# Optimization experiments

Hardware: AMD Instinct MI355X
Metric: run time of the kernel (lower is better)

Reference implementation:

```python
import jax, jax.numpy as jnp
import numpy as np

N = 1_000_000
DIM = 128
NUM_GRAPHS = 4096


def setup_inputs() -> dict:
    key = jax.random.key(0)
    kx, kq, kb = jax.random.split(key, 3)
    x = jax.random.normal(kx, (N, DIM), dtype=jnp.float32)
    query = jax.random.normal(kq, (DIM,), dtype=jnp.float32) * 0.02
    batch = jnp.sort(jax.random.randint(kb, (N,), 0, NUM_GRAPHS, dtype=jnp.int64))
    return {"x": x, "query": query, "batch": batch}


def reference(x, query, batch):
    # scores: [N] dot of each node feature with the learned query vector
    scores = jnp.einsum("nd,d->n", x, query)
    # segment-wise numerically-stable softmax over nodes belonging to each graph
    seg_max = jax.ops.segment_max(scores, batch, num_segments=NUM_GRAPHS)
    ex = jnp.exp(scores - seg_max[batch])  # [N]
    seg_sum = jax.ops.segment_sum(ex, batch, num_segments=NUM_GRAPHS)
    weights = ex / seg_sum[batch]  # [N]
    # weighted scatter-add pooling -> [num_graphs, dim]
    pooled = jax.ops.segment_sum(weights[:, None] * x, batch, num_segments=NUM_GRAPHS)
    return pooled
```

## Files before the change

kernel.cpp:

```cpp
#include <hip/hip_runtime.h>
#include <math.h>

#define DIM 128
#define CHUNK 4
#define STREAMS 8
#define STRIDE (STREAMS)
#define ROUND (STREAMS * CHUNK)

__device__ __forceinline__ int lower_bound_i(const int* __restrict__ b, int n, int key) {
    int lo = 0, hi = n;
    while (lo < hi) {
        int mid = (lo + hi) >> 1;
        if (b[mid] < key) lo = mid + 1; else hi = mid;
    }
    return lo;
}

__global__ __launch_bounds__(256) void attnpool_kernel(
    const float* __restrict__ x, const float* __restrict__ q,
    const int* __restrict__ batch, float* __restrict__ out, int n)
{
    const int g    = blockIdx.x;
    const int tid  = threadIdx.x;
    const int wave = tid >> 6;
    const int lane = tid & 63;
    const int half = lane >> 5;
    const int hl   = lane & 31;
    const int sid  = wave * 2 + half;

    const int lo = lower_bound_i(batch, n, g);
    const int hi = lower_bound_i(batch, n, g + 1);

    const float4 qf = *(const float4*)(q + hl * 4);

    float  m = -INFINITY;
    float  l = 0.f;
    float4 o = make_float4(0.f, 0.f, 0.f, 0.f);

    const int i0 = lo + sid;
    const float4 z = make_float4(0.f, 0.f, 0.f, 0.f);

    float4 cur[CHUNK];
    #pragma unroll
    for (int j = 0; j < CHUNK; ++j) {
        const int ii = i0 + j * STRIDE;
        cur[j] = (ii < hi) ? *(const float4*)(x + (size_t)ii * DIM + hl * 4) : z;
    }

    for (int base = i0; base < hi; base += ROUND) {
        float4 nxt[CHUNK];
        #pragma unroll
        for (int j = 0; j < CHUNK; ++j) {
            const int ii = base + ROUND + j * STRIDE;
            nxt[j] = (ii < hi) ? *(const float4*)(x + (size_t)ii * DIM + hl * 4) : z;
        }

        float s[CHUNK];
        #pragma unroll
        for (int j = 0; j < CHUNK; ++j)
            s[j] = cur[j].x * qf.x + cur[j].y * qf.y + cur[j].z * qf.z + cur[j].w * qf.w;

        #pragma unroll
        for (int d = 16; d >= 1; d >>= 1) {
            #pragma unroll
            for (int j = 0; j < CHUNK; ++j)
                s[j] += __shfl_xor(s[j], d);
        }

        #pragma unroll
        for (int j = 0; j < CHUNK; ++j)
            if (base + j * STRIDE >= hi) s[j] = -INFINITY;

        const float smax = fmaxf(fmaxf(s[0], s[1]), fmaxf(s[2], s[3]));
        if (smax > m) {
            const float a = __expf(m - smax);
            l *= a;
            o.x *= a; o.y *= a; o.z *= a; o.w *= a;
            m = smax;
        }

        #pragma unroll
        for (int j = 0; j < CHUNK; ++j) {
            const float p = (base + j * STRIDE < hi) ? __expf(s[j] - m) : 0.f;
            l += p;
            o.x += p * cur[j].x; o.y += p * cur[j].y;
            o.z += p * cur[j].z; o.w += p * cur[j].w;
        }

        #pragma unroll
        for (int j = 0; j < CHUNK; ++j) cur[j] = nxt[j];
    }

    __shared__ float sm_m[STREAMS];
    __shared__ float sm_l[STREAMS];
    __shared__ float sm_o[STREAMS * DIM];
    if (hl == 0) { sm_m[sid] = m; sm_l[sid] = l; }
    *(float4*)(sm_o + sid * DIM + hl * 4) = o;
    __syncthreads();

    if (tid < DIM) {
        float M = -INFINITY;
        #pragma unroll
        for (int h = 0; h < STREAMS; ++h)
            if (sm_l[h] > 0.f && sm_m[h] > M) M = sm_m[h];
        float L = 0.f, O = 0.f;
        #pragma unroll
        for (int h = 0; h < STREAMS; ++h) {
            if (sm_l[h] > 0.f) {
                const float c = __expf(sm_m[h] - M);
                L += c * sm_l[h];
                O += c * sm_o[h * DIM + tid];
            }
        }
        out[(size_t)g * DIM + tid] = (L > 0.f) ? (O / L) : 0.f;
    }
}

extern "C" void kernel_launch(void* const* d_in, const int* in_sizes, int n_in,
                              void* d_out, int out_size, void* d_ws, size_t ws_size,
                              hipStream_t stream) {
    const float* x     = (const float*)d_in[0];
    const float* q     = (const float*)d_in[1];
    const int*   batch = (const int*)d_in[2];
    float*       out   = (float*)d_out;
    const int n          = in_sizes[0] / DIM;
    const int num_graphs = out_size / DIM;
    attnpool_kernel<<<num_graphs, 256, 0, stream>>>(x, q, batch, out, n);
}
```

Measured before the change: 676.1 us.

## Use nontemporal loads, drop register prefetch, split main loop and tail

Removes the manual next-chunk register prefetch in favour of straight nontemporal vector loads. The loop is split into an unguarded full-chunk main loop and a per-row tail loop, which removes the bounds masks. Launch bounds now request 8 blocks per CU to raise occupancy, and the output uses nontemporal stores. Dropping the software prefetch relies on occupancy to hide memory latency and could expose load latency per iteration.

```diff
diff --git a/kernel.cpp b/kernel.cpp
--- a/kernel.cpp
+++ b/kernel.cpp
@@ -6,6 +6,8 @@
 #define STREAMS 8
 #define STRIDE (STREAMS)
 #define ROUND (STREAMS * CHUNK)
+
+typedef float v4f __attribute__((ext_vector_type(4)));
 
 __device__ __forceinline__ int lower_bound_i(const int* __restrict__ b, int n, int key) {
     int lo = 0, hi = n;
@@ -16,7 +18,7 @@
     return lo;
 }
 
-__global__ __launch_bounds__(256) void attnpool_kernel(
+__global__ __launch_bounds__(256, 8) void attnpool_kernel(
     const float* __restrict__ x, const float* __restrict__ q,
     const int* __restrict__ batch, float* __restrict__ out, int n)
 {
@@ -37,23 +39,14 @@
     float  l = 0.f;
     float4 o = make_float4(0.f, 0.f, 0.f, 0.f);
 
-    const int i0 = lo + sid;
-    const float4 z = make_float4(0.f, 0.f, 0.f, 0.f);
+    const float* xb = x + hl * 4;
+    int i = lo + sid;
 
-    float4 cur[CHUNK];
-    #pragma unroll
-    for (int j = 0; j < CHUNK; ++j) {
-        const int ii = i0 + j * STRIDE;
-        cur[j] = (ii < hi) ? *(const float4*)(x + (size_t)ii * DIM + hl * 4) : z;
-    }
-
-    for (int base = i0; base < hi; base += ROUND) {
-        float4 nxt[CHUNK];
+    while (i + (CHUNK - 1) * STRIDE < hi) {
+        v4f cur[CHUNK];
         #pragma unroll
-        for (int j = 0; j < CHUNK; ++j) {
-            const int ii = base + ROUND + j * STRIDE;
-            nxt[j] = (ii < hi) ? *(const float4*)(x + (size_t)ii * DIM + hl * 4) : z;
-        }
+        for (int j = 0; j < CHUNK; ++j)
+            cur[j] = __builtin_nontemporal_load((const v4f*)(xb + (size_t)(i + j * STRIDE) * DIM));
 
         float s[CHUNK];
         #pragma unroll
@@ -67,10 +60,6 @@
                 s[j] += __shfl_xor(s[j], d);
         }
 
-        #pragma unroll
-        for (int j = 0; j < CHUNK; ++j)
-            if (base + j * STRIDE >= hi) s[j] = -INFINITY;
-
         const float smax = fmaxf(fmaxf(s[0], s[1]), fmaxf(s[2], s[3]));
         if (smax > m) {
             const float a = __expf(m - smax);
@@ -81,21 +70,39 @@
 
         #pragma unroll
         for (int j = 0; j < CHUNK; ++j) {
-            const float p = (base + j * STRIDE < hi) ? __expf(s[j] - m) : 0.f;
+            const float p = __expf(s[j] - m);
             l += p;
             o.x += p * cur[j].x; o.y += p * cur[j].y;
             o.z += p * cur[j].z; o.w += p * cur[j].w;
         }
 
+        i += ROUND;
+    }
+
+    for (; i < hi; i += STRIDE) {
+        const v4f xv = __builtin_nontemporal_load((const v4f*)(xb + (size_t)i * DIM));
+        float s = xv.x * qf.x + xv.y * qf.y + xv.z * qf.z + xv.w * qf.w;
         #pragma unroll
-        for (int j = 0; j < CHUNK; ++j) cur[j] = nxt[j];
+        for (int d = 16; d >= 1; d >>= 1) s += __shfl_xor(s, d);
+        if (s > m) {
+            const float a = __expf(m - s);
+            l = l * a + 1.f;
+            o.x = o.x * a + xv.x; o.y = o.y * a + xv.y;
+            o.z = o.z * a + xv.z; o.w = o.w * a + xv.w;
+            m = s;
+        } else {
+            const float p = __expf(s - m);
+            l += p;
+            o.x += p * xv.x; o.y += p * xv.y;
+            o.z += p * xv.z; o.w += p * xv.w;
+        }
     }
 
     __shared__ float sm_m[STREAMS];
     __shared__ float sm_l[STREAMS];
     __shared__ float sm_o[STREAMS * DIM];
     if (hl == 0) { sm_m[sid] = m; sm_l[sid] = l; }
-    *(float4*)(sm_o + sid * DIM + hl * 4) = o;
+    *(float4*)(sm_o + sid * DIM + hl * 4) = make_float4(o.x, o.y, o.z, o.w);
     __syncthreads();
 
     if (tid < DIM) {
@@ -112,7 +119,7 @@
                 O += c * sm_o[h * DIM + tid];
             }
         }
-        out[(size_t)g * DIM + tid] = (L > 0.f) ? (O / L) : 0.f;
+        __builtin_nontemporal_store((L > 0.f) ? (O / L) : 0.f, out + (size_t)g * DIM + tid);
     }
 }
 
```

After: 629.9 us. -6.8%, faster.
